# Kernel optimization log

Measured on AMD Instinct MI355X. Metric: run time of the kernel, lower is better.

The kernel has to match this reference:

```python
import jax, jax.numpy as jnp
import numpy as np

WS = 8      # window size
NH = 8      # num heads
DIM = 128   # channels


def _rel_index(ws):
    # Swin relative-position index, identical to the torch buffer construction
    coords = np.stack(np.meshgrid(np.arange(ws), np.arange(ws), indexing='ij')).reshape(2, -1)
    rel = (coords[:, :, None] - coords[:, None, :]).transpose(1, 2, 0)  # [N,N,2]
    rel[:, :, 0] += ws - 1
    rel[:, :, 1] += ws - 1
    rel[:, :, 0] *= 2 * ws - 1
    return rel.sum(-1)  # [N,N] in [0, (2ws-1)^2)


def setup_inputs() -> dict:
    key = jax.random.key(0)
    ks = jax.random.split(key, 4)
    return {
        'x': jax.random.normal(ks[0], (2, DIM, 256, 256), jnp.float32),
        'qkv_w': jax.random.normal(ks[1], (3 * DIM, DIM), jnp.float32) * 0.02,
        'qkv_b': jnp.zeros((3 * DIM,), jnp.float32),
        'proj_w': jax.random.normal(ks[2], (DIM, DIM), jnp.float32) * 0.02,
        'proj_b': jnp.zeros((DIM,), jnp.float32),
        'rel_bias': jax.random.normal(ks[3], ((2 * WS - 1) ** 2, NH), jnp.float32) * 0.02,
        'rel_index': jnp.asarray(_rel_index(WS), jnp.int32),
    }


def reference(x, qkv_w, qkv_b, proj_w, proj_b, rel_bias, rel_index):
    B, C, H, W = x.shape
    ws, nh = WS, NH
    hd = C // nh
    scale = hd ** -0.5
    pad_h = (-H) % ws
    pad_w = (-W) % ws
    x = jnp.pad(x, ((0, 0), (0, 0), (0, pad_h), (0, pad_w)))
    Hp, Wp = H + pad_h, W + pad_w
    N = ws * ws
    # window partition -> tokens [B*nWh*nWw, N, C] (channels-last; 1x1 conv == linear)
    xw = x.reshape(B, C, Hp // ws, ws, Wp // ws, ws)
    xw = xw.transpose(0, 2, 4, 3, 5, 1).reshape(-1, N, C)
    qkv = xw @ qkv_w.T + qkv_b                      # [Bw, N, 3C]
    q, k, v = jnp.split(qkv, 3, axis=-1)

    def heads(t):  # [Bw, N, C] -> [Bw, nh, N, hd]
        return t.reshape(t.shape[0], N, nh, hd).transpose(0, 2, 1, 3)

    q, k, v = heads(q), heads(k), heads(v)
    attn = jnp.einsum('bhid,bhjd->bhij', q, k) * scale   # [Bw, nh, N, N]
    bias = rel_bias[rel_index].transpose(2, 0, 1)        # [nh, N, N]
    attn = jax.nn.softmax(attn + bias[None], axis=-1)
    out = jnp.einsum('bhij,bhjd->bhid', attn, v)         # [Bw, nh, N, hd]
    out = out.transpose(0, 2, 1, 3).reshape(-1, N, C)    # [Bw, N, C]
    # window un-partition -> [B, C, Hp, Wp]
    out = out.reshape(B, Hp // ws, Wp // ws, ws, ws, C)
    out = out.transpose(0, 5, 1, 3, 2, 4).reshape(B, C, Hp, Wp)
    out = out[:, :, :H, :W]
    # proj: 1x1 conv
    return jnp.einsum('bchw,oc->bohw', out, proj_w) + proj_b[None, :, None, None]
```

## Files before the change

kernel.cpp:

```cpp
#include <hip/hip_runtime.h>

#define CDIM 128
#define NHEADS 8
#define HD 16
#define NTOK 64
#define HW 65536
#define XSTR 136
#define VSTR 72

typedef short s8v __attribute__((ext_vector_type(8)));
typedef short s4v __attribute__((ext_vector_type(4)));
typedef float f4v __attribute__((ext_vector_type(4)));

static __device__ __forceinline__ short f2bf(float f) {
    unsigned u = __float_as_uint(f);
    u += 0x7FFFu + ((u >> 16) & 1u);
    return (short)(u >> 16);
}

__global__ __launch_bounds__(256) void pack_w_kernel(
    const float* __restrict__ qkv_w, const float* __restrict__ proj_w,
    short* __restrict__ wpk)
{
    int idx = blockIdx.x * 256 + threadIdx.x;
    int lane = idx & 63, kc = (idx >> 6) & 3, ob = idx >> 8;
    int row = (ob < 24) ? ob * 16 + (lane & 15) : (ob - 24) * 16 + (lane & 15);
    int col = kc * 32 + (lane >> 4) * 8;
    const float* src = ((ob < 24) ? qkv_w : proj_w) + (size_t)row * CDIM + col;
    float sc = (ob < 8) ? 0.25f : 1.0f;
    float4 f0 = *(const float4*)src;
    float4 f1 = *(const float4*)(src + 4);
    s8v r;
    r[0] = f2bf(f0.x * sc); r[1] = f2bf(f0.y * sc);
    r[2] = f2bf(f0.z * sc); r[3] = f2bf(f0.w * sc);
    r[4] = f2bf(f1.x * sc); r[5] = f2bf(f1.y * sc);
    r[6] = f2bf(f1.z * sc); r[7] = f2bf(f1.w * sc);
    *(s8v*)&wpk[(size_t)idx * 8] = r;
}

__global__ __launch_bounds__(256) void pack_b_kernel(
    const float* __restrict__ rel_bias, const int* __restrict__ rel_index,
    float* __restrict__ biasf)
{
    int idx = blockIdx.x * 256 + threadIdx.x;
    int lane = idx & 63, nt = (idx >> 6) & 3, mt = (idx >> 8) & 3, h = idx >> 10;
    int j  = nt * 16 + (lane & 15);
    int i0 = mt * 16 + (lane >> 4) * 4;
    f4v v;
    #pragma unroll
    for (int r = 0; r < 4; ++r)
        v[r] = rel_bias[rel_index[(i0 + r) * 64 + j] * NHEADS + h];
    *(f4v*)&biasf[(size_t)idx * 4] = v;
}

__global__ __launch_bounds__(256) void winattn_kernel(
    const float* __restrict__ x, const float* __restrict__ qkv_b,
    const float* __restrict__ proj_b, const short* __restrict__ wpk,
    const float* __restrict__ biasf, float* __restrict__ out)
{
    __shared__ __align__(16) short xs[NTOK * XSTR];
    __shared__ __align__(16) short qs[NTOK * XSTR];
    __shared__ __align__(16) short ks[NTOK * XSTR];
    __shared__ __align__(16) short vt[CDIM * VSTR];
    __shared__ __align__(16) short ps[4 * 16 * VSTR];

    const int tid  = threadIdx.x;
    const int lane = tid & 63;
    const int wv   = tid >> 6;
    const int qd   = lane >> 4;
    const int l15  = lane & 15;

    const int wid = (blockIdx.x & 7) * 256 + (blockIdx.x >> 3);
    const int b   = wid >> 10;
    const int wy  = (wid >> 5) & 31, wx = wid & 31;
    const int h0  = wy * 8, w0 = wx * 8;
    const float* xb = x + (size_t)b * CDIM * HW;

    for (int idx = tid; idx < CDIM * 16; idx += 256) {
        int c = idx >> 4, tq = idx & 15;
        int t0 = tq * 4;
        float4 f = *(const float4*)&xb[(size_t)c * HW + (h0 + (t0 >> 3)) * 256 + w0 + (t0 & 7)];
        xs[(t0 + 0) * XSTR + c] = f2bf(f.x);
        xs[(t0 + 1) * XSTR + c] = f2bf(f.y);
        xs[(t0 + 2) * XSTR + c] = f2bf(f.z);
        xs[(t0 + 3) * XSTR + c] = f2bf(f.w);
    }
    __syncthreads();

    {
        s8v X[4][4];
        #pragma unroll
        for (int tb = 0; tb < 4; ++tb)
            #pragma unroll
            for (int kc = 0; kc < 4; ++kc)
                X[tb][kc] = *(const s8v*)&xs[(tb * 16 + l15) * XSTR + kc * 32 + qd * 8];

        const s8v* wf = (const s8v*)wpk;
        #pragma unroll
        for (int i = 0; i < 6; ++i) {
            const int ob = wv * 6 + i;
            s8v W[4];
            #pragma unroll
            for (int kc = 0; kc < 4; ++kc) W[kc] = wf[(ob * 4 + kc) * 64 + lane];
            if (ob < 16) {
                const int o0 = ob * 16 + qd * 4;
                float4 qb4 = *(const float4*)&qkv_b[o0];
                const float bsc = (ob < 8) ? 0.25f : 1.0f;
                float qb[4] = {qb4.x * bsc, qb4.y * bsc, qb4.z * bsc, qb4.w * bsc};
                #pragma unroll
                for (int tb = 0; tb < 4; ++tb) {
                    f4v acc = {0.f, 0.f, 0.f, 0.f};
                    #pragma unroll
                    for (int kc = 0; kc < 4; ++kc)
                        acc = __builtin_amdgcn_mfma_f32_16x16x32_bf16(W[kc], X[tb][kc], acc, 0, 0, 0);
                    const int t = tb * 16 + l15;
                    s4v pk;
                    #pragma unroll
                    for (int r = 0; r < 4; ++r) pk[r] = f2bf(acc[r] + qb[r]);
                    if (o0 < 128) *(s4v*)&qs[t * XSTR + o0]       = pk;
                    else          *(s4v*)&ks[t * XSTR + o0 - 128] = pk;
                }
            } else {
                const int o = (ob - 16) * 16 + l15;
                const float vb = qkv_b[256 + o];
                #pragma unroll
                for (int tb = 0; tb < 4; ++tb) {
                    f4v acc = {0.f, 0.f, 0.f, 0.f};
                    #pragma unroll
                    for (int kc = 0; kc < 4; ++kc)
                        acc = __builtin_amdgcn_mfma_f32_16x16x32_bf16(X[tb][kc], W[kc], acc, 0, 0, 0);
                    const int t0 = tb * 16 + qd * 4;
                    s4v pk;
                    #pragma unroll
                    for (int r = 0; r < 4; ++r) pk[r] = f2bf(acc[r] + vb);
                    *(s4v*)&vt[o * VSTR + t0] = pk;
                }
            }
        }
    }
    __syncthreads();

    short* os = xs;
    const s8v z8 = {};
    #pragma unroll
    for (int pass = 0; pass < 2; ++pass) {
        const int h = wv + pass * 4;
        s8v kf[4];
        #pragma unroll
        for (int nt = 0; nt < 4; ++nt)
            kf[nt] = (qd < 2) ? *(const s8v*)&ks[(nt * 16 + l15) * XSTR + h * HD + qd * 8] : z8;
        s8v vf[2];
        #pragma unroll
        for (int kc = 0; kc < 2; ++kc)
            vf[kc] = *(const s8v*)&vt[(h * HD + l15) * VSTR + kc * 32 + qd * 8];

        #pragma unroll
        for (int mt = 0; mt < 4; ++mt) {
            s8v qf = (qd < 2) ? *(const s8v*)&qs[(mt * 16 + l15) * XSTR + h * HD + qd * 8] : z8;
            float sv[4][4];
            #pragma unroll
            for (int nt = 0; nt < 4; ++nt) {
                f4v s = {0.f, 0.f, 0.f, 0.f};
                s = __builtin_amdgcn_mfma_f32_16x16x32_bf16(qf, kf[nt], s, 0, 0, 0);
                f4v bf = *(const f4v*)&biasf[(size_t)(((h * 4 + mt) * 4 + nt) * 64 + lane) * 4];
                #pragma unroll
                for (int r = 0; r < 4; ++r) sv[nt][r] = s[r] + bf[r];
            }
            float inv[4];
            #pragma unroll
            for (int r = 0; r < 4; ++r) {
                float mx = fmaxf(fmaxf(sv[0][r], sv[1][r]), fmaxf(sv[2][r], sv[3][r]));
                #pragma unroll
                for (int off = 1; off < 16; off <<= 1) mx = fmaxf(mx, __shfl_xor(mx, off, 64));
                float sm = 0.f;
                #pragma unroll
                for (int nt = 0; nt < 4; ++nt) { sv[nt][r] = __expf(sv[nt][r] - mx); sm += sv[nt][r]; }
                #pragma unroll
                for (int off = 1; off < 16; off <<= 1) sm += __shfl_xor(sm, off, 64);
                inv[r] = 1.f / sm;
            }
            short* pw = &ps[wv * 16 * VSTR];
            #pragma unroll
            for (int nt = 0; nt < 4; ++nt) {
                s4v pk;
                #pragma unroll
                for (int r = 0; r < 4; ++r) pk[r] = f2bf(sv[nt][r]);
                pw[(qd * 4 + 0) * VSTR + nt * 16 + l15] = pk[0];
                pw[(qd * 4 + 1) * VSTR + nt * 16 + l15] = pk[1];
                pw[(qd * 4 + 2) * VSTR + nt * 16 + l15] = pk[2];
                pw[(qd * 4 + 3) * VSTR + nt * 16 + l15] = pk[3];
            }
            s8v pa0 = *(const s8v*)&pw[l15 * VSTR + 0 * 32 + qd * 8];
            s8v pa1 = *(const s8v*)&pw[l15 * VSTR + 1 * 32 + qd * 8];
            f4v O = {0.f, 0.f, 0.f, 0.f};
            O = __builtin_amdgcn_mfma_f32_16x16x32_bf16(pa0, vf[0], O, 0, 0, 0);
            O = __builtin_amdgcn_mfma_f32_16x16x32_bf16(pa1, vf[1], O, 0, 0, 0);
            #pragma unroll
            for (int r = 0; r < 4; ++r)
                os[(mt * 16 + qd * 4 + r) * XSTR + h * HD + l15] = f2bf(O[r] * inv[r]);
        }
    }
    __syncthreads();

    {
        s8v A[4][4];
        #pragma unroll
        for (int mt = 0; mt < 4; ++mt)
            #pragma unroll
            for (int kc = 0; kc < 4; ++kc)
                A[mt][kc] = *(const s8v*)&os[(mt * 16 + l15) * XSTR + kc * 32 + qd * 8];

        const s8v* wf = (const s8v*)wpk;
        s8v B[2][4];
        float pb2[2]; int o2[2];
        #pragma unroll
        for (int nt = 0; nt < 2; ++nt) {
            const int ob = 24 + wv * 2 + nt;
            o2[nt] = (wv * 2 + nt) * 16 + l15;
            pb2[nt] = proj_b[o2[nt]];
            #pragma unroll
            for (int kc = 0; kc < 4; ++kc) B[nt][kc] = wf[(ob * 4 + kc) * 64 + lane];
        }
        #pragma unroll
        for (int mt = 0; mt < 4; ++mt) {
            const int t0 = mt * 16 + qd * 4;
            const int pix = (h0 + (t0 >> 3)) * 256 + w0 + (t0 & 7);
            #pragma unroll
            for (int nt = 0; nt < 2; ++nt) {
                f4v acc = {0.f, 0.f, 0.f, 0.f};
                #pragma unroll
                for (int kc = 0; kc < 4; ++kc)
                    acc = __builtin_amdgcn_mfma_f32_16x16x32_bf16(A[mt][kc], B[nt][kc], acc, 0, 0, 0);
                float4 v = make_float4(acc[0] + pb2[nt], acc[1] + pb2[nt],
                                       acc[2] + pb2[nt], acc[3] + pb2[nt]);
                *(float4*)&out[((size_t)(b * CDIM + o2[nt])) * HW + pix] = v;
            }
        }
    }
}

extern "C" void kernel_launch(void* const* d_in, const int* in_sizes, int n_in,
                              void* d_out, int out_size, void* d_ws, size_t ws_size,
                              hipStream_t stream) {
    const float* x        = (const float*)d_in[0];
    const float* qkv_w    = (const float*)d_in[1];
    const float* qkv_b    = (const float*)d_in[2];
    const float* proj_w   = (const float*)d_in[3];
    const float* proj_b   = (const float*)d_in[4];
    const float* rel_bias = (const float*)d_in[5];
    const int*   rel_index= (const int*)d_in[6];
    float* out = (float*)d_out;

    short* wpk   = (short*)d_ws;
    float* biasf = (float*)((char*)d_ws + 131072);

    pack_w_kernel<<<32, 256, 0, stream>>>(qkv_w, proj_w, wpk);
    pack_b_kernel<<<32, 256, 0, stream>>>(rel_bias, rel_index, biasf);
    winattn_kernel<<<2048, 256, 0, stream>>>(x, qkv_b, proj_b, wpk, biasf, out);
}
```

Before: 195.6 us.

## Restructure window attention per-head to cut LDS footprint and raise occupancy

Each wave now computes K, V and Q for its own two heads. V stays in registers through a small per-wave scratch buffer, and Q overwrites the x tile after a barrier, so the separate qs, vt and ps shared buffers are removed. The x staging store uses an XOR-swizzled column layout to reduce LDS bank conflicts. Scores are computed transposed (K·Q) so the softmax reduction needs only two cross-lane shuffles, and the bias pack layout is changed to match. Launch bounds now request 3 blocks per CU, which may force register spilling in exchange for higher occupancy.

```diff
diff --git a/kernel.cpp b/kernel.cpp
--- a/kernel.cpp
+++ b/kernel.cpp
@@ -43,26 +43,24 @@
     float* __restrict__ biasf)
 {
     int idx = blockIdx.x * 256 + threadIdx.x;
-    int lane = idx & 63, nt = (idx >> 6) & 3, mt = (idx >> 8) & 3, h = idx >> 10;
-    int j  = nt * 16 + (lane & 15);
-    int i0 = mt * 16 + (lane >> 4) * 4;
+    int lane = idx & 63, nt = (idx >> 6) & 3, mq = (idx >> 8) & 3, h = idx >> 10;
+    int tq  = mq * 16 + (lane & 15);
+    int tk0 = nt * 16 + (lane >> 4) * 4;
     f4v v;
     #pragma unroll
     for (int r = 0; r < 4; ++r)
-        v[r] = rel_bias[rel_index[(i0 + r) * 64 + j] * NHEADS + h];
+        v[r] = rel_bias[rel_index[tq * 64 + tk0 + r] * NHEADS + h];
     *(f4v*)&biasf[(size_t)idx * 4] = v;
 }
 
-__global__ __launch_bounds__(256) void winattn_kernel(
+__global__ __launch_bounds__(256, 3) void winattn_kernel(
     const float* __restrict__ x, const float* __restrict__ qkv_b,
     const float* __restrict__ proj_b, const short* __restrict__ wpk,
     const float* __restrict__ biasf, float* __restrict__ out)
 {
     __shared__ __align__(16) short xs[NTOK * XSTR];
-    __shared__ __align__(16) short qs[NTOK * XSTR];
     __shared__ __align__(16) short ks[NTOK * XSTR];
-    __shared__ __align__(16) short vt[CDIM * VSTR];
-    __shared__ __align__(16) short ps[4 * 16 * VSTR];
+    __shared__ __align__(16) short vsc[4 * 2 * 16 * VSTR];
 
     const int tid  = threadIdx.x;
     const int lane = tid & 63;
@@ -76,128 +74,159 @@
     const int h0  = wy * 8, w0 = wx * 8;
     const float* xb = x + (size_t)b * CDIM * HW;
 
-    for (int idx = tid; idx < CDIM * 16; idx += 256) {
-        int c = idx >> 4, tq = idx & 15;
-        int t0 = tq * 4;
+    #pragma unroll
+    for (int it = 0; it < 8; ++it) {
+        const int g   = it * 4 + wv;
+        const int cg  = g & 15, tqg = g >> 4;
+        const int c   = cg * 8 + (lane & 7);
+        const int tq  = tqg * 8 + ((lane >> 3) & 7);
+        const int t0  = tq * 4;
         float4 f = *(const float4*)&xb[(size_t)c * HW + (h0 + (t0 >> 3)) * 256 + w0 + (t0 & 7)];
-        xs[(t0 + 0) * XSTR + c] = f2bf(f.x);
-        xs[(t0 + 1) * XSTR + c] = f2bf(f.y);
-        xs[(t0 + 2) * XSTR + c] = f2bf(f.z);
-        xs[(t0 + 3) * XSTR + c] = f2bf(f.w);
+        const int col = ((cg ^ (tq & 7)) << 3) | (c & 7);
+        xs[(t0 + 0) * XSTR + col] = f2bf(f.x);
+        xs[(t0 + 1) * XSTR + col] = f2bf(f.y);
+        xs[(t0 + 2) * XSTR + col] = f2bf(f.z);
+        xs[(t0 + 3) * XSTR + col] = f2bf(f.w);
     }
     __syncthreads();
 
+    s8v vf[2][2];
     {
         s8v X[4][4];
         #pragma unroll
         for (int tb = 0; tb < 4; ++tb)
             #pragma unroll
-            for (int kc = 0; kc < 4; ++kc)
-                X[tb][kc] = *(const s8v*)&xs[(tb * 16 + l15) * XSTR + kc * 32 + qd * 8];
+            for (int kc = 0; kc < 4; ++kc) {
+                const int gr = ((4 * kc + qd) ^ ((4 * tb + (l15 >> 2)) & 7)) << 3;
+                X[tb][kc] = *(const s8v*)&xs[(tb * 16 + l15) * XSTR + gr];
+            }
 
         const s8v* wf = (const s8v*)wpk;
-        #pragma unroll
-        for (int i = 0; i < 6; ++i) {
-            const int ob = wv * 6 + i;
+
+        #pragma unroll
+        for (int hp = 0; hp < 2; ++hp) {
+            const int h = wv + hp * 4;
+            const int ob = 8 + h;
             s8v W[4];
             #pragma unroll
             for (int kc = 0; kc < 4; ++kc) W[kc] = wf[(ob * 4 + kc) * 64 + lane];
-            if (ob < 16) {
-                const int o0 = ob * 16 + qd * 4;
-                float4 qb4 = *(const float4*)&qkv_b[o0];
-                const float bsc = (ob < 8) ? 0.25f : 1.0f;
-                float qb[4] = {qb4.x * bsc, qb4.y * bsc, qb4.z * bsc, qb4.w * bsc};
-                #pragma unroll
-                for (int tb = 0; tb < 4; ++tb) {
-                    f4v acc = {0.f, 0.f, 0.f, 0.f};
-                    #pragma unroll
-                    for (int kc = 0; kc < 4; ++kc)
-                        acc = __builtin_amdgcn_mfma_f32_16x16x32_bf16(W[kc], X[tb][kc], acc, 0, 0, 0);
-                    const int t = tb * 16 + l15;
-                    s4v pk;
-                    #pragma unroll
-                    for (int r = 0; r < 4; ++r) pk[r] = f2bf(acc[r] + qb[r]);
-                    if (o0 < 128) *(s4v*)&qs[t * XSTR + o0]       = pk;
-                    else          *(s4v*)&ks[t * XSTR + o0 - 128] = pk;
-                }
-            } else {
-                const int o = (ob - 16) * 16 + l15;
-                const float vb = qkv_b[256 + o];
-                #pragma unroll
-                for (int tb = 0; tb < 4; ++tb) {
-                    f4v acc = {0.f, 0.f, 0.f, 0.f};
-                    #pragma unroll
-                    for (int kc = 0; kc < 4; ++kc)
-                        acc = __builtin_amdgcn_mfma_f32_16x16x32_bf16(X[tb][kc], W[kc], acc, 0, 0, 0);
-                    const int t0 = tb * 16 + qd * 4;
-                    s4v pk;
-                    #pragma unroll
-                    for (int r = 0; r < 4; ++r) pk[r] = f2bf(acc[r] + vb);
-                    *(s4v*)&vt[o * VSTR + t0] = pk;
-                }
-            }
-        }
-    }
-    __syncthreads();
+            float4 kb = *(const float4*)&qkv_b[128 + h * 16 + qd * 4];
+            float kbr[4] = {kb.x, kb.y, kb.z, kb.w};
+            #pragma unroll
+            for (int tb = 0; tb < 4; ++tb) {
+                f4v acc = {0.f, 0.f, 0.f, 0.f};
+                #pragma unroll
+                for (int kc = 0; kc < 4; ++kc)
+                    acc = __builtin_amdgcn_mfma_f32_16x16x32_bf16(W[kc], X[tb][kc], acc, 0, 0, 0);
+                s4v pk;
+                #pragma unroll
+                for (int r = 0; r < 4; ++r) pk[r] = f2bf(acc[r] + kbr[r]);
+                *(s4v*)&ks[(tb * 16 + l15) * XSTR + h * 16 + qd * 4] = pk;
+            }
+        }
+
+        #pragma unroll
+        for (int hp = 0; hp < 2; ++hp) {
+            const int h = wv + hp * 4;
+            const int ob = 16 + h;
+            short* vw = &vsc[(wv * 2 + hp) * 16 * VSTR];
+            s8v W[4];
+            #pragma unroll
+            for (int kc = 0; kc < 4; ++kc) W[kc] = wf[(ob * 4 + kc) * 64 + lane];
+            const float vb = qkv_b[256 + h * 16 + l15];
+            #pragma unroll
+            for (int tb = 0; tb < 4; ++tb) {
+                f4v acc = {0.f, 0.f, 0.f, 0.f};
+                #pragma unroll
+                for (int kc = 0; kc < 4; ++kc)
+                    acc = __builtin_amdgcn_mfma_f32_16x16x32_bf16(X[tb][kc], W[kc], acc, 0, 0, 0);
+                s4v pk;
+                #pragma unroll
+                for (int r = 0; r < 4; ++r) pk[r] = f2bf(acc[r] + vb);
+                *(s4v*)&vw[l15 * VSTR + tb * 16 + qd * 4] = pk;
+            }
+            vf[hp][0] = *(const s8v*)&vw[l15 * VSTR + qd * 8];
+            vf[hp][1] = *(const s8v*)&vw[l15 * VSTR + 32 + qd * 8];
+        }
+
+        __syncthreads();
+
+        #pragma unroll
+        for (int hp = 0; hp < 2; ++hp) {
+            const int h = wv + hp * 4;
+            const int ob = h;
+            s8v W[4];
+            #pragma unroll
+            for (int kc = 0; kc < 4; ++kc) W[kc] = wf[(ob * 4 + kc) * 64 + lane];
+            float4 qb = *(const float4*)&qkv_b[h * 16 + qd * 4];
+            float qbr[4] = {qb.x * 0.25f, qb.y * 0.25f, qb.z * 0.25f, qb.w * 0.25f};
+            #pragma unroll
+            for (int tb = 0; tb < 4; ++tb) {
+                f4v acc = {0.f, 0.f, 0.f, 0.f};
+                #pragma unroll
+                for (int kc = 0; kc < 4; ++kc)
+                    acc = __builtin_amdgcn_mfma_f32_16x16x32_bf16(W[kc], X[tb][kc], acc, 0, 0, 0);
+                s4v pk;
+                #pragma unroll
+                for (int r = 0; r < 4; ++r) pk[r] = f2bf(acc[r] + qbr[r]);
+                *(s4v*)&xs[(tb * 16 + l15) * XSTR + h * 16 + qd * 4] = pk;
+            }
+        }
+    }
 
     short* os = xs;
     const s8v z8 = {};
     #pragma unroll
-    for (int pass = 0; pass < 2; ++pass) {
-        const int h = wv + pass * 4;
+    for (int hp = 0; hp < 2; ++hp) {
+        const int h = wv + hp * 4;
         s8v kf[4];
         #pragma unroll
-        for (int nt = 0; nt < 4; ++nt)
-            kf[nt] = (qd < 2) ? *(const s8v*)&ks[(nt * 16 + l15) * XSTR + h * HD + qd * 8] : z8;
-        s8v vf[2];
-        #pragma unroll
-        for (int kc = 0; kc < 2; ++kc)
-            vf[kc] = *(const s8v*)&vt[(h * HD + l15) * VSTR + kc * 32 + qd * 8];
-
-        #pragma unroll
-        for (int mt = 0; mt < 4; ++mt) {
-            s8v qf = (qd < 2) ? *(const s8v*)&qs[(mt * 16 + l15) * XSTR + h * HD + qd * 8] : z8;
-            float sv[4][4];
+        for (int nt = 0; nt < 4; ++nt) {
+            s8v kr = *(const s8v*)&ks[(nt * 16 + l15) * XSTR + h * 16 + (qd & 1) * 8];
+            kf[nt] = (qd < 2) ? kr : z8;
+        }
+        #pragma unroll
+        for (int mq = 0; mq < 4; ++mq) {
+            s8v qf = *(const s8v*)&xs[(mq * 16 + l15) * XSTR + h * 16 + (qd & 1) * 8];
+            f4v sv[4];
             #pragma unroll
             for (int nt = 0; nt < 4; ++nt) {
                 f4v s = {0.f, 0.f, 0.f, 0.f};
-                s = __builtin_amdgcn_mfma_f32_16x16x32_bf16(qf, kf[nt], s, 0, 0, 0);
-                f4v bf = *(const f4v*)&biasf[(size_t)(((h * 4 + mt) * 4 + nt) * 64 + lane) * 4];
-                #pragma unroll
-                for (int r = 0; r < 4; ++r) sv[nt][r] = s[r] + bf[r];
-            }
-            float inv[4];
-            #pragma unroll
-            for (int r = 0; r < 4; ++r) {
-                float mx = fmaxf(fmaxf(sv[0][r], sv[1][r]), fmaxf(sv[2][r], sv[3][r]));
-                #pragma unroll
-                for (int off = 1; off < 16; off <<= 1) mx = fmaxf(mx, __shfl_xor(mx, off, 64));
-                float sm = 0.f;
-                #pragma unroll
-                for (int nt = 0; nt < 4; ++nt) { sv[nt][r] = __expf(sv[nt][r] - mx); sm += sv[nt][r]; }
-                #pragma unroll
-                for (int off = 1; off < 16; off <<= 1) sm += __shfl_xor(sm, off, 64);
-                inv[r] = 1.f / sm;
-            }
-            short* pw = &ps[wv * 16 * VSTR];
+                s = __builtin_amdgcn_mfma_f32_16x16x32_bf16(kf[nt], qf, s, 0, 0, 0);
+                f4v bf = *(const f4v*)&biasf[(size_t)(((h * 4 + mq) * 4 + nt) * 64 + lane) * 4];
+                sv[nt] = s + bf;
+            }
+            f4v a;
+            #pragma unroll
+            for (int r = 0; r < 4; ++r)
+                a[r] = fmaxf(fmaxf(sv[0][r], sv[1][r]), fmaxf(sv[2][r], sv[3][r]));
+            float mx = fmaxf(fmaxf(a[0], a[1]), fmaxf(a[2], a[3]));
+            mx = fmaxf(mx, __shfl_xor(mx, 16, 64));
+            mx = fmaxf(mx, __shfl_xor(mx, 32, 64));
+            float sm = 0.f;
+            #pragma unroll
+            for (int nt = 0; nt < 4; ++nt)
+                #pragma unroll
+                for (int r = 0; r < 4; ++r) { sv[nt][r] = __expf(sv[nt][r] - mx); sm += sv[nt][r]; }
+            sm += __shfl_xor(sm, 16, 64);
+            sm += __shfl_xor(sm, 32, 64);
+            const float inv = 1.f / sm;
+            short* pw = &vsc[(wv * 2 + (mq & 1)) * 16 * VSTR];
             #pragma unroll
             for (int nt = 0; nt < 4; ++nt) {
                 s4v pk;
                 #pragma unroll
-                for (int r = 0; r < 4; ++r) pk[r] = f2bf(sv[nt][r]);
-                pw[(qd * 4 + 0) * VSTR + nt * 16 + l15] = pk[0];
-                pw[(qd * 4 + 1) * VSTR + nt * 16 + l15] = pk[1];
-                pw[(qd * 4 + 2) * VSTR + nt * 16 + l15] = pk[2];
-                pw[(qd * 4 + 3) * VSTR + nt * 16 + l15] = pk[3];
-            }
-            s8v pa0 = *(const s8v*)&pw[l15 * VSTR + 0 * 32 + qd * 8];
-            s8v pa1 = *(const s8v*)&pw[l15 * VSTR + 1 * 32 + qd * 8];
+                for (int r = 0; r < 4; ++r) pk[r] = f2bf(sv[nt][r] * inv);
+                *(s4v*)&pw[l15 * VSTR + nt * 16 + qd * 4] = pk;
+            }
+            s8v pa0 = *(const s8v*)&pw[l15 * VSTR + qd * 8];
+            s8v pa1 = *(const s8v*)&pw[l15 * VSTR + 32 + qd * 8];
             f4v O = {0.f, 0.f, 0.f, 0.f};
-            O = __builtin_amdgcn_mfma_f32_16x16x32_bf16(pa0, vf[0], O, 0, 0, 0);
-            O = __builtin_amdgcn_mfma_f32_16x16x32_bf16(pa1, vf[1], O, 0, 0, 0);
+            O = __builtin_amdgcn_mfma_f32_16x16x32_bf16(pa0, vf[hp][0], O, 0, 0, 0);
+            O = __builtin_amdgcn_mfma_f32_16x16x32_bf16(pa1, vf[hp][1], O, 0, 0, 0);
             #pragma unroll
             for (int r = 0; r < 4; ++r)
-                os[(mt * 16 + qd * 4 + r) * XSTR + h * HD + l15] = f2bf(O[r] * inv[r]);
+                os[(mq * 16 + qd * 4 + r) * XSTR + h * HD + l15] = f2bf(O[r]);
         }
     }
     __syncthreads();
```

After: 170.7 us. 1.15x faster.
